# Kernel tuning notes

Hardware: AMD Instinct MI355X
Metric: run time of the kernel (lower is better)

The kernel has to match this reference:

```python
import jax, jax.numpy as jnp
import numpy as np

NEG_SLOPE = 0.2  # leakyrelu negative_slope from init

def _lrelu(x):
    return jax.nn.leaky_relu(x, NEG_SLOPE)

def setup_inputs() -> dict:
    key = jax.random.key(0)
    k1, k2, k3 = jax.random.split(key, 3)
    B, N, Fin, Fout = 8, 2048, 128, 64
    x = jax.random.normal(k1, (B, N, Fin), dtype=jnp.float32)
    W = jax.random.normal(k2, (Fin, Fout), dtype=jnp.float32) * (1.414 / np.sqrt(Fin))
    a = jax.random.normal(k3, (2 * Fout, 1), dtype=jnp.float32) * 0.1
    return {"x": x, "W": W, "a": a}

def reference(x, W, a):
    # x: (B, N, Fin), W: (Fin, Fout), a: (2*Fout, 1)
    Fout = W.shape[1]
    h = jnp.matmul(x, W)  # (B, N, Fout)
    a1 = a[:Fout, 0]      # attends to source node i
    a2 = a[Fout:, 0]      # attends to target node j
    # e[b,i,j] = leakyrelu(h[b,i]@a1 + h[b,j]@a2); avoids O(N^2*2F) repeat+cat
    s1 = jnp.einsum('bnf,f->bn', h, a1)  # (B, N)
    s2 = jnp.einsum('bnf,f->bn', h, a2)  # (B, N)
    e = _lrelu(s1[:, :, None] + s2[:, None, :])  # (B, N, N)
    attention = jax.nn.softmax(e, axis=1)  # softmax over dim=1, as in source
    # dropout in eval mode: identity
    h_prime = jnp.matmul(attention, h)  # (B, N, Fout)
    return _lrelu(h_prime)
```

## Files before the change

kernel.cpp:

```cpp
#include <hip/hip_runtime.h>
#include <math.h>

#define B 8
#define N 2048
#define NP1 2049
#define FIN 128
#define FOUT 64
#define NS 0.2f
#define K 2048
#define KP1 2049
#define NCH 64
#define CHS 32

__device__ __forceinline__ int bucketOf(float v) {
  int q = (int)floorf((v + 8.0f) * 128.0f);
  return min(max(q, 0), K - 1);
}

__device__ __forceinline__ int wscan_add_i(int v, int lane) {
#pragma unroll
  for (int off = 1; off < 64; off <<= 1) {
    int o = __shfl_up(v, off, 64);
    v += (lane >= off) ? o : 0;
  }
  return v;
}
__device__ __forceinline__ float wscan_add_f(float v, int lane) {
#pragma unroll
  for (int off = 1; off < 64; off <<= 1) {
    float o = __shfl_up(v, off, 64);
    v += (lane >= off) ? o : 0.f;
  }
  return v;
}

#define RPB 32
__global__ __launch_bounds__(256, 2) void k_hs(
    const float* __restrict__ x, const float* __restrict__ W,
    const float* __restrict__ a, float* __restrict__ h,
    float* __restrict__ s1, float* __restrict__ s2) {
  __shared__ float xs[RPB * FIN];
  const int row0 = blockIdx.x * RPB;
  const int lane = threadIdx.x & 63;
  const int wv = threadIdx.x >> 6;

  {
    const float4* src = (const float4*)(x + (size_t)row0 * FIN);
    float4* dst = (float4*)xs;
#pragma unroll
    for (int t = 0; t < 4; ++t)
      dst[threadIdx.x + 256 * t] = src[threadIdx.x + 256 * t];
  }

  float w[FIN];
#pragma unroll
  for (int k = 0; k < FIN; ++k) w[k] = W[k * FOUT + lane];
  const float a1 = a[lane];
  const float a2 = a[FOUT + lane];
  __syncthreads();

  for (int n = 0; n < 8; ++n) {
    const int r = wv * 8 + n;
    const float* xr = xs + r * FIN;
    float ac0 = 0.f, ac1 = 0.f, ac2 = 0.f, ac3 = 0.f;
#pragma unroll
    for (int k4 = 0; k4 < FIN; k4 += 4) {
      float4 xv = *(const float4*)(xr + k4);
      ac0 = fmaf(xv.x, w[k4 + 0], ac0);
      ac1 = fmaf(xv.y, w[k4 + 1], ac1);
      ac2 = fmaf(xv.z, w[k4 + 2], ac2);
      ac3 = fmaf(xv.w, w[k4 + 3], ac3);
    }
    const float acc = (ac0 + ac1) + (ac2 + ac3);
    const int row = row0 + r;
    h[(size_t)row * FOUT + lane] = acc;

    float v1 = acc * a1;
    float v2 = acc * a2;
#pragma unroll
    for (int off = 32; off > 0; off >>= 1) {
      v1 += __shfl_xor(v1, off, 64);
      v2 += __shfl_xor(v2, off, 64);
    }
    if (lane == 0) {
      s1[row] = v1;
      s2[row] = v2;
    }
  }
}

__global__ __launch_bounds__(1024) void k_bucket(
    const float* __restrict__ s1, const float* __restrict__ s2,
    int* __restrict__ start1, float* __restrict__ elemS1,
    float* __restrict__ elemU, float* __restrict__ elemUq,
    float* __restrict__ slotPrefU, float* __restrict__ slotPrefQ,
    int* __restrict__ start2, float* __restrict__ elemS2,
    int* __restrict__ idx2) {
  __shared__ int cnt[K];
  __shared__ int cur[K];
  __shared__ float eS[N];
  __shared__ float eU[N];
  __shared__ float eQ[N];
  __shared__ int eJ[N];
  __shared__ int wtI[16];
  __shared__ float wtU[16], wtQ[16];

  const int type = blockIdx.x & 1;
  const int b = blockIdx.x >> 1;
  const int tid = threadIdx.x;
  const int lane = tid & 63;
  const int wv = tid >> 6;
  const float* key = (type ? s2 : s1) + b * N;

  cnt[tid] = 0;
  cnt[tid + 1024] = 0;
  __syncthreads();
  const float k0 = key[tid], k1 = key[tid + 1024];
  const int q0 = bucketOf(k0), q1 = bucketOf(k1);
  atomicAdd(&cnt[q0], 1);
  atomicAdd(&cnt[q1], 1);
  __syncthreads();

  {
    const int c0 = cnt[2 * tid], c1 = cnt[2 * tid + 1];
    const int loc = c0 + c1;
    const int incl = wscan_add_i(loc, lane);
    if (lane == 63) wtI[wv] = incl;
    __syncthreads();
    int cross = 0;
#pragma unroll
    for (int w = 0; w < 16; ++w) cross += (w < wv) ? wtI[w] : 0;
    const int ex = cross + incl - loc;
    cnt[2 * tid] = ex;       cnt[2 * tid + 1] = ex + c0;
    cur[2 * tid] = ex;       cur[2 * tid + 1] = ex + c0;
  }
  __syncthreads();

  if (type == 0) {
    int sl = atomicAdd(&cur[q0], 1);
    eS[sl] = k0; eU[sl] = expf(k0); eQ[sl] = expf(NS * k0);
    sl = atomicAdd(&cur[q1], 1);
    eS[sl] = k1; eU[sl] = expf(k1); eQ[sl] = expf(NS * k1);
  } else {
    int sl = atomicAdd(&cur[q0], 1);
    eS[sl] = k0; eJ[sl] = tid;
    sl = atomicAdd(&cur[q1], 1);
    eS[sl] = k1; eJ[sl] = tid + 1024;
  }
  __syncthreads();

  if (type == 1) {
    elemS2[b * N + tid] = eS[tid];
    elemS2[b * N + tid + 1024] = eS[tid + 1024];
    idx2[b * N + tid] = eJ[tid];
    idx2[b * N + tid + 1024] = eJ[tid + 1024];
    start2[b * KP1 + tid] = cnt[tid];
    start2[b * KP1 + tid + 1024] = cnt[tid + 1024];
    if (tid == 0) start2[b * KP1 + K] = N;
    return;
  }

  elemS1[b * N + tid] = eS[tid];
  elemS1[b * N + tid + 1024] = eS[tid + 1024];
  elemU[b * N + tid] = eU[tid];
  elemU[b * N + tid + 1024] = eU[tid + 1024];
  elemUq[b * N + tid] = eQ[tid];
  elemUq[b * N + tid + 1024] = eQ[tid + 1024];
  start1[b * KP1 + tid] = cnt[tid];
  start1[b * KP1 + tid + 1024] = cnt[tid + 1024];
  if (tid == 0) start1[b * KP1 + K] = N;

  const float u0 = eU[2 * tid], u1 = eU[2 * tid + 1];
  const float g0 = eQ[2 * tid], g1 = eQ[2 * tid + 1];
  const float locU = u0 + u1, locQ = g0 + g1;
  const float iU = wscan_add_f(locU, lane);
  const float iQ = wscan_add_f(locQ, lane);
  if (lane == 63) { wtU[wv] = iU; wtQ[wv] = iQ; }
  __syncthreads();
  float crU = 0.f, crQ = 0.f, totU = 0.f, totQ = 0.f;
#pragma unroll
  for (int w = 0; w < 16; ++w) {
    const float au = wtU[w], aq = wtQ[w];
    crU += (w < wv) ? au : 0.f;
    crQ += (w < wv) ? aq : 0.f;
    totU += au; totQ += aq;
  }
  const float exU = crU + iU - locU, exQ = crQ + iQ - locQ;
  slotPrefU[b * NP1 + 2 * tid] = exU;
  slotPrefU[b * NP1 + 2 * tid + 1] = exU + u0;
  slotPrefQ[b * NP1 + 2 * tid] = exQ;
  slotPrefQ[b * NP1 + 2 * tid + 1] = exQ + g0;
  if (tid == 0) { slotPrefU[b * NP1 + N] = totU; slotPrefQ[b * NP1 + N] = totQ; }
}

__global__ void k_z(const float* __restrict__ elemS1, const float* __restrict__ elemU,
                    const float* __restrict__ elemUq, const float* __restrict__ slotPrefU,
                    const float* __restrict__ slotPrefQ, const int* __restrict__ start1,
                    const float* __restrict__ elemS2, float2* __restrict__ AB) {
  const int g = blockIdx.x * 256 + threadIdx.x;
  const int b = g >> 11;
  const int s = g & (N - 1);
  const float s2v = elemS2[b * N + s];
  const float t = -s2v;
  const int q = bucketOf(t);
  const int sb = start1[b * KP1 + q], se = start1[b * KP1 + q + 1];
  float Pu = slotPrefU[b * NP1 + sb];
  float Pq = slotPrefQ[b * NP1 + sb];
  for (int i = sb; i < se; ++i) {
    const bool lt = elemS1[b * N + i] < t;
    Pu += lt ? elemU[b * N + i] : 0.f;
    Pq += lt ? elemUq[b * N + i] : 0.f;
  }
  const float totU = slotPrefU[b * NP1 + N];
  const float E = expf(s2v), Eq = expf(NS * s2v);
  const float Z = E * (totU - Pu) + Eq * Pq;
  AB[b * N + s] = make_float2(E / Z, Eq / Z);
}

__global__ void k_scan1(const float2* __restrict__ AB,
                        const float* __restrict__ h, const int* __restrict__ idx2,
                        float* __restrict__ hperm,
                        float* __restrict__ ctA, float* __restrict__ ctB) {
  const int b = blockIdx.x >> 4;
  const int chunk = (blockIdx.x & 15) * 4 + (threadIdx.x >> 6);
  const int f = threadIdx.x & 63;
  const int s0 = chunk * CHS;

  float ta = 0.f, tb = 0.f;
#pragma unroll
  for (int g = 0; g < 2; ++g) {
    float hv[16]; float2 ab[16];
#pragma unroll
    for (int rr = 0; rr < 16; ++rr) {
      const int s = s0 + g * 16 + rr;
      const int j = idx2[b * N + s];
      hv[rr] = h[((size_t)b * N + j) * FOUT + f];
      ab[rr] = AB[b * N + s];
    }
#pragma unroll
    for (int rr = 0; rr < 16; ++rr) {
      const int s = s0 + g * 16 + rr;
      hperm[((size_t)b * N + s) * FOUT + f] = hv[rr];
      ta = fmaf(ab[rr].x, hv[rr], ta);
      tb = fmaf(ab[rr].y, hv[rr], tb);
    }
  }
  ctA[(b * NCH + chunk) * FOUT + f] = ta;
  ctB[(b * NCH + chunk) * FOUT + f] = tb;
}

__global__ __launch_bounds__(256) void k_scan2(
    const float2* __restrict__ AB, const float* __restrict__ hperm,
    const float* __restrict__ ctA, const float* __restrict__ ctB,
    float* __restrict__ SA, float* __restrict__ PB) {
  __shared__ float cA[NCH * FOUT];
  __shared__ float cB[NCH * FOUT];
  const int b = blockIdx.x >> 4;
  const int chunk = (blockIdx.x & 15) * 4 + (threadIdx.x >> 6);
  const int f = threadIdx.x & 63;
  const int s0 = chunk * CHS;

  for (int t = threadIdx.x; t < NCH * FOUT; t += 256) {
    cA[t] = ctA[b * NCH * FOUT + t];
    cB[t] = ctB[b * NCH * FOUT + t];
  }
  __syncthreads();

  float offA = 0.f, offB = 0.f;
#pragma unroll 8
  for (int c2 = 0; c2 < NCH; ++c2) {
    const float va = cA[c2 * FOUT + f];
    const float vb = cB[c2 * FOUT + f];
    if (c2 > chunk) offA += va;
    if (c2 < chunk) offB += vb;
  }

  float run = offB;
#pragma unroll
  for (int g = 0; g < 2; ++g) {
    float hv[16]; float2 ab[16];
#pragma unroll
    for (int rr = 0; rr < 16; ++rr) {
      const int s = s0 + g * 16 + rr;
      hv[rr] = hperm[((size_t)b * N + s) * FOUT + f];
      ab[rr] = AB[b * N + s];
    }
#pragma unroll
    for (int rr = 0; rr < 16; ++rr) {
      run = fmaf(ab[rr].y, hv[rr], run);
      PB[((size_t)b * NP1 + s0 + g * 16 + rr + 1) * FOUT + f] = run;
    }
  }
  run = offA;
#pragma unroll
  for (int g = 1; g >= 0; --g) {
    float hv[16]; float2 ab[16];
#pragma unroll
    for (int rr = 0; rr < 16; ++rr) {
      const int s = s0 + g * 16 + rr;
      hv[rr] = hperm[((size_t)b * N + s) * FOUT + f];
      ab[rr] = AB[b * N + s];
    }
#pragma unroll
    for (int rr = 15; rr >= 0; --rr) {
      run = fmaf(ab[rr].x, hv[rr], run);
      SA[((size_t)b * NP1 + s0 + g * 16 + rr) * FOUT + f] = run;
    }
  }
  if (chunk == 0) {
    PB[((size_t)b * NP1 + 0) * FOUT + f] = 0.f;
    SA[((size_t)b * NP1 + N) * FOUT + f] = 0.f;
  }
}

__global__ void k_out(const float* __restrict__ s1,
                      const int* __restrict__ start2,
                      const float* __restrict__ elemS2,
                      const float2* __restrict__ AB,
                      const float* __restrict__ hperm,
                      const float* __restrict__ SA,
                      const float* __restrict__ PB,
                      float* __restrict__ out) {
  const int wv = threadIdx.x >> 6;
  const int lane = threadIdx.x & 63;
  const int row = blockIdx.x * 4 + wv;
  const int b = row >> 11;
  const float s1v = s1[row];
  const float t = -s1v;
  const int q = bucketOf(t);
  const int sb = start2[b * KP1 + q];
  const int se = start2[b * KP1 + q + 1];

  float sa = SA[((size_t)b * NP1 + se) * FOUT + lane];
  float pb = PB[((size_t)b * NP1 + sb) * FOUT + lane];
  for (int s = sb; s < se; ++s) {
    const float s2v = elemS2[b * N + s];
    const float2 ab = AB[b * N + s];
    const float hv = hperm[((size_t)b * N + s) * FOUT + lane];
    if (s2v >= t) sa = fmaf(ab.x, hv, sa);
    else          pb = fmaf(ab.y, hv, pb);
  }
  const float uu = expf(s1v), uqv = expf(NS * s1v);
  const float v = uu * sa + uqv * pb;
  out[(size_t)row * FOUT + lane] = v >= 0.f ? v : NS * v;
}

extern "C" void kernel_launch(void* const* d_in, const int* in_sizes, int n_in,
                              void* d_out, int out_size, void* d_ws, size_t ws_size,
                              hipStream_t stream) {
  const float* x = (const float*)d_in[0];
  const float* W = (const float*)d_in[1];
  const float* a = (const float*)d_in[2];
  float* out = (float*)d_out;

  float* ws = (float*)d_ws;
  float* h = ws;
  float* hperm = h + (size_t)B * N * FOUT;
  float* s1 = hperm + (size_t)B * N * FOUT;
  float* s2 = s1 + B * N;
  float* elemS1 = s2 + B * N;
  float* elemU = elemS1 + B * N;
  float* elemUq = elemU + B * N;
  float* elemS2 = elemUq + B * N;
  float* slotPrefU = elemS2 + B * N;
  float* slotPrefQ = slotPrefU + B * NP1;
  float2* AB = (float2*)(slotPrefQ + B * NP1);
  int* idx2 = (int*)(AB + (size_t)B * N);
  int* start1 = idx2 + B * N;
  int* start2 = start1 + B * KP1;
  float* ctA = (float*)(start2 + B * KP1);
  float* ctB = ctA + (size_t)B * NCH * FOUT;
  float* SA = ctB + (size_t)B * NCH * FOUT;
  float* PB = SA + (size_t)B * NP1 * FOUT;

  k_hs<<<B * N / RPB, 256, 0, stream>>>(x, W, a, h, s1, s2);
  k_bucket<<<2 * B, 1024, 0, stream>>>(s1, s2, start1, elemS1, elemU, elemUq,
                                       slotPrefU, slotPrefQ, start2, elemS2, idx2);
  k_z<<<B * (N / 256), 256, 0, stream>>>(elemS1, elemU, elemUq, slotPrefU,
                                         slotPrefQ, start1, elemS2, AB);
  k_scan1<<<B * 16, 256, 0, stream>>>(AB, h, idx2, hperm, ctA, ctB);
  k_scan2<<<B * 16, 256, 0, stream>>>(AB, hperm, ctA, ctB, SA, PB);
  k_out<<<B * N / 4, 256, 0, stream>>>(s1, start2, elemS2, AB, hperm, SA, PB, out);
}
```

Before: 55.42 us.

## Fuse normalizer and two scan passes into one kernel with per-batch spin barrier

Merges the Z/normalizer kernel and both scan kernels into a single launch. Each wave computes A/B coefficients for its own 32 rows and shares them via lane shuffles. Gathered h values stay in registers, so hperm and AB are not re-read. Chunk totals are synchronized across the 16 blocks of a batch with an atomic counter spin barrier instead of a kernel boundary. This removes two launches and redundant global traffic, but it relies on all 128 blocks being co-resident, and the counter reset happens inside the preceding kernel.

New measurement: 61.69 us. +11.3%, slower.

```diff
diff --git a/kernel.cpp b/kernel.cpp
--- a/kernel.cpp
+++ b/kernel.cpp
@@ -95,7 +95,7 @@
     float* __restrict__ elemU, float* __restrict__ elemUq,
     float* __restrict__ slotPrefU, float* __restrict__ slotPrefQ,
     int* __restrict__ start2, float* __restrict__ elemS2,
-    int* __restrict__ idx2) {
+    int* __restrict__ idx2, int* __restrict__ done) {
   __shared__ int cnt[K];
   __shared__ int cur[K];
   __shared__ float eS[N];
@@ -111,6 +111,8 @@
   const int lane = tid & 63;
   const int wv = tid >> 6;
   const float* key = (type ? s2 : s1) + b * N;
+
+  if (blockIdx.x == 0 && tid < B) done[tid] = 0;
 
   cnt[tid] = 0;
   cnt[tid + 1024] = 0;
@@ -193,72 +195,75 @@
   if (tid == 0) { slotPrefU[b * NP1 + N] = totU; slotPrefQ[b * NP1 + N] = totQ; }
 }
 
-__global__ void k_z(const float* __restrict__ elemS1, const float* __restrict__ elemU,
-                    const float* __restrict__ elemUq, const float* __restrict__ slotPrefU,
-                    const float* __restrict__ slotPrefQ, const int* __restrict__ start1,
-                    const float* __restrict__ elemS2, float2* __restrict__ AB) {
-  const int g = blockIdx.x * 256 + threadIdx.x;
-  const int b = g >> 11;
-  const int s = g & (N - 1);
-  const float s2v = elemS2[b * N + s];
-  const float t = -s2v;
-  const int q = bucketOf(t);
-  const int sb = start1[b * KP1 + q], se = start1[b * KP1 + q + 1];
-  float Pu = slotPrefU[b * NP1 + sb];
-  float Pq = slotPrefQ[b * NP1 + sb];
-  for (int i = sb; i < se; ++i) {
-    const bool lt = elemS1[b * N + i] < t;
-    Pu += lt ? elemU[b * N + i] : 0.f;
-    Pq += lt ? elemUq[b * N + i] : 0.f;
-  }
-  const float totU = slotPrefU[b * NP1 + N];
-  const float E = expf(s2v), Eq = expf(NS * s2v);
-  const float Z = E * (totU - Pu) + Eq * Pq;
-  AB[b * N + s] = make_float2(E / Z, Eq / Z);
-}
-
-__global__ void k_scan1(const float2* __restrict__ AB,
-                        const float* __restrict__ h, const int* __restrict__ idx2,
-                        float* __restrict__ hperm,
-                        float* __restrict__ ctA, float* __restrict__ ctB) {
-  const int b = blockIdx.x >> 4;
-  const int chunk = (blockIdx.x & 15) * 4 + (threadIdx.x >> 6);
-  const int f = threadIdx.x & 63;
-  const int s0 = chunk * CHS;
-
-  float ta = 0.f, tb = 0.f;
-#pragma unroll
-  for (int g = 0; g < 2; ++g) {
-    float hv[16]; float2 ab[16];
-#pragma unroll
-    for (int rr = 0; rr < 16; ++rr) {
-      const int s = s0 + g * 16 + rr;
-      const int j = idx2[b * N + s];
-      hv[rr] = h[((size_t)b * N + j) * FOUT + f];
-      ab[rr] = AB[b * N + s];
-    }
-#pragma unroll
-    for (int rr = 0; rr < 16; ++rr) {
-      const int s = s0 + g * 16 + rr;
-      hperm[((size_t)b * N + s) * FOUT + f] = hv[rr];
-      ta = fmaf(ab[rr].x, hv[rr], ta);
-      tb = fmaf(ab[rr].y, hv[rr], tb);
-    }
-  }
-  ctA[(b * NCH + chunk) * FOUT + f] = ta;
-  ctB[(b * NCH + chunk) * FOUT + f] = tb;
-}
-
-__global__ __launch_bounds__(256) void k_scan2(
-    const float2* __restrict__ AB, const float* __restrict__ hperm,
-    const float* __restrict__ ctA, const float* __restrict__ ctB,
-    float* __restrict__ SA, float* __restrict__ PB) {
+__global__ __launch_bounds__(256) void k_scan(
+    const float* __restrict__ elemS1, const float* __restrict__ elemU,
+    const float* __restrict__ elemUq, const float* __restrict__ slotPrefU,
+    const float* __restrict__ slotPrefQ, const int* __restrict__ start1,
+    const float* __restrict__ elemS2, const int* __restrict__ idx2,
+    const float* __restrict__ h, float2* __restrict__ AB,
+    float* __restrict__ hperm, float* __restrict__ ctA, float* __restrict__ ctB,
+    float* __restrict__ SA, float* __restrict__ PB, int* __restrict__ done) {
   __shared__ float cA[NCH * FOUT];
   __shared__ float cB[NCH * FOUT];
   const int b = blockIdx.x >> 4;
   const int chunk = (blockIdx.x & 15) * 4 + (threadIdx.x >> 6);
   const int f = threadIdx.x & 63;
   const int s0 = chunk * CHS;
+
+  float Aval = 0.f, Bval = 0.f;
+  if (f < 32) {
+    const int s = s0 + f;
+    const float s2v = elemS2[b * N + s];
+    const float t = -s2v;
+    const int q = bucketOf(t);
+    const int sb = start1[b * KP1 + q], se = start1[b * KP1 + q + 1];
+    float Pu = slotPrefU[b * NP1 + sb];
+    float Pq = slotPrefQ[b * NP1 + sb];
+    for (int i = sb; i < se; ++i) {
+      const bool lt = elemS1[b * N + i] < t;
+      Pu += lt ? elemU[b * N + i] : 0.f;
+      Pq += lt ? elemUq[b * N + i] : 0.f;
+    }
+    const float totU = slotPrefU[b * NP1 + N];
+    const float E = expf(s2v), Eq = expf(NS * s2v);
+    const float Z = E * (totU - Pu) + Eq * Pq;
+    Aval = E / Z;
+    Bval = Eq / Z;
+    AB[b * N + s] = make_float2(Aval, Bval);
+  }
+
+  float hv[CHS];
+#pragma unroll
+  for (int g = 0; g < 2; ++g) {
+#pragma unroll
+    for (int rr = 0; rr < 16; ++rr) {
+      const int s = s0 + g * 16 + rr;
+      const int j = idx2[b * N + s];
+      hv[g * 16 + rr] = h[((size_t)b * N + j) * FOUT + f];
+    }
+  }
+  float ta = 0.f, tb = 0.f;
+#pragma unroll
+  for (int rr = 0; rr < CHS; ++rr) {
+    hperm[((size_t)b * N + s0 + rr) * FOUT + f] = hv[rr];
+    const float av = __shfl(Aval, rr, 64);
+    const float bv = __shfl(Bval, rr, 64);
+    ta = fmaf(av, hv[rr], ta);
+    tb = fmaf(bv, hv[rr], tb);
+  }
+  ctA[(b * NCH + chunk) * FOUT + f] = ta;
+  ctB[(b * NCH + chunk) * FOUT + f] = tb;
+
+  __syncthreads();
+  if (threadIdx.x == 0) {
+    __threadfence();
+    atomicAdd(&done[b], 1);
+    while (atomicAdd(&done[b], 0) < 16) {
+      __builtin_amdgcn_s_sleep(2);
+    }
+    __threadfence();
+  }
+  __syncthreads();
 
   for (int t = threadIdx.x; t < NCH * FOUT; t += 256) {
     cA[t] = ctA[b * NCH * FOUT + t];
@@ -277,35 +282,17 @@
 
   float run = offB;
 #pragma unroll
-  for (int g = 0; g < 2; ++g) {
-    float hv[16]; float2 ab[16];
-#pragma unroll
-    for (int rr = 0; rr < 16; ++rr) {
-      const int s = s0 + g * 16 + rr;
-      hv[rr] = hperm[((size_t)b * N + s) * FOUT + f];
-      ab[rr] = AB[b * N + s];
-    }
-#pragma unroll
-    for (int rr = 0; rr < 16; ++rr) {
-      run = fmaf(ab[rr].y, hv[rr], run);
-      PB[((size_t)b * NP1 + s0 + g * 16 + rr + 1) * FOUT + f] = run;
-    }
+  for (int rr = 0; rr < CHS; ++rr) {
+    const float bv = __shfl(Bval, rr, 64);
+    run = fmaf(bv, hv[rr], run);
+    PB[((size_t)b * NP1 + s0 + rr + 1) * FOUT + f] = run;
   }
   run = offA;
 #pragma unroll
-  for (int g = 1; g >= 0; --g) {
-    float hv[16]; float2 ab[16];
-#pragma unroll
-    for (int rr = 0; rr < 16; ++rr) {
-      const int s = s0 + g * 16 + rr;
-      hv[rr] = hperm[((size_t)b * N + s) * FOUT + f];
-      ab[rr] = AB[b * N + s];
-    }
-#pragma unroll
-    for (int rr = 15; rr >= 0; --rr) {
-      run = fmaf(ab[rr].x, hv[rr], run);
-      SA[((size_t)b * NP1 + s0 + g * 16 + rr) * FOUT + f] = run;
-    }
+  for (int rr = CHS - 1; rr >= 0; --rr) {
+    const float av = __shfl(Aval, rr, 64);
+    run = fmaf(av, hv[rr], run);
+    SA[((size_t)b * NP1 + s0 + rr) * FOUT + f] = run;
   }
   if (chunk == 0) {
     PB[((size_t)b * NP1 + 0) * FOUT + f] = 0.f;
@@ -372,13 +359,14 @@
   float* ctB = ctA + (size_t)B * NCH * FOUT;
   float* SA = ctB + (size_t)B * NCH * FOUT;
   float* PB = SA + (size_t)B * NP1 * FOUT;
+  int* done = (int*)(PB + (size_t)B * NP1 * FOUT);
 
   k_hs<<<B * N / RPB, 256, 0, stream>>>(x, W, a, h, s1, s2);
   k_bucket<<<2 * B, 1024, 0, stream>>>(s1, s2, start1, elemS1, elemU, elemUq,
-                                       slotPrefU, slotPrefQ, start2, elemS2, idx2);
-  k_z<<<B * (N / 256), 256, 0, stream>>>(elemS1, elemU, elemUq, slotPrefU,
-                                         slotPrefQ, start1, elemS2, AB);
-  k_scan1<<<B * 16, 256, 0, stream>>>(AB, h, idx2, hperm, ctA, ctB);
-  k_scan2<<<B * 16, 256, 0, stream>>>(AB, hperm, ctA, ctB, SA, PB);
+                                       slotPrefU, slotPrefQ, start2, elemS2,
+                                       idx2, done);
+  k_scan<<<B * 16, 256, 0, stream>>>(elemS1, elemU, elemUq, slotPrefU,
+                                     slotPrefQ, start1, elemS2, idx2, h, AB,
+                                     hperm, ctA, ctB, SA, PB, done);
   k_out<<<B * N / 4, 256, 0, stream>>>(s1, start2, elemS2, AB, hperm, SA, PB, out);
 }
```
